# Optimization experiments

Measured on AMD Instinct MI355X. Metric: run time of the kernel, lower is better.

Reference implementation:

```python
import jax, jax.numpy as jnp
import numpy as np

B = 262144
MA = [128, 128]
MB = [128, 128]


def krone_linear(x_a, x_b, wa, wb, ba, bb):
    # slice inputs to each branch's in_features (torch slices the wider branch)
    ia, ib = wa.shape[1], wb.shape[1]
    x_a = x_a[:, :ia]
    x_b = x_b[:, :ib]
    h_a = x_a @ wa.T + ba
    h_b = x_b @ wb.T + bb
    # zero-pad the narrower output so both branches share a width (static shapes)
    oa, ob = wa.shape[0], wb.shape[0]
    if oa > ob:
        h_b = jnp.pad(h_b, ((0, 0), (0, oa - ob)))
    elif ob > oa:
        h_a = jnp.pad(h_a, ((0, 0), (0, ob - oa)))
    return h_a, h_b


def krone_softmax(x_a, x_b, fa, fb):
    x_a = x_a[:, :fa]
    x_b = x_b[:, :fb]
    # vectorized per-row Kronecker product: kron(a, b)[i*fb + j] = a[i]*b[j]
    y = (x_a[:, :, None] * x_b[:, None, :]).reshape(x_a.shape[0], fa * fb)
    return jax.nn.softmax(y, axis=1)


def setup_inputs() -> dict:
    key = jax.random.key(0)
    ks = jax.random.split(key, 13)
    s = 0.1
    inp = {
        "x": jax.random.normal(ks[0], (2, B, 2), dtype=jnp.float32),
        "w1a": jax.random.normal(ks[1], (MA[0], 2), dtype=jnp.float32) * s,
        "w1b": jax.random.normal(ks[2], (MB[0], 2), dtype=jnp.float32) * s,
        "b1a": jax.random.normal(ks[3], (MA[0],), dtype=jnp.float32) * s,
        "b1b": jax.random.normal(ks[4], (MB[0],), dtype=jnp.float32) * s,
        "w2a": jax.random.normal(ks[5], (MA[1], MA[0]), dtype=jnp.float32) * s,
        "w2b": jax.random.normal(ks[6], (MB[1], MB[0]), dtype=jnp.float32) * s,
        "b2a": jax.random.normal(ks[7], (MA[1],), dtype=jnp.float32) * s,
        "b2b": jax.random.normal(ks[8], (MB[1],), dtype=jnp.float32) * s,
        "w3a": jax.random.normal(ks[9], (1, MA[1]), dtype=jnp.float32) * s,
        "w3b": jax.random.normal(ks[10], (3, MB[1]), dtype=jnp.float32) * s,
        "b3a": jax.random.normal(ks[11], (1,), dtype=jnp.float32) * s,
        "b3b": jax.random.normal(ks[12], (3,), dtype=jnp.float32) * s,
    }
    return inp


def reference(x, w1a, w1b, b1a, b1b, w2a, w2b, b2a, b2b, w3a, w3b, b3a, b3b):
    x_a, x_b = x[0], x[1]
    h_a, h_b = krone_linear(x_a, x_b, w1a, w1b, b1a, b1b)
    h_a, h_b = jax.nn.relu(h_a), jax.nn.relu(h_b)
    h_a, h_b = krone_linear(h_a, h_b, w2a, w2b, b2a, b2b)
    h_a, h_b = jax.nn.relu(h_a), jax.nn.relu(h_b)
    h_a, h_b = krone_linear(h_a, h_b, w3a, w3b, b3a, b3b)
    return krone_softmax(h_a, h_b, 1, 3)
```

## Files before the change

kernel.cpp:

```cpp
#include <hip/hip_runtime.h>
#include <hip/hip_bf16.h>


#define BTOT 262144
#define NBLK (BTOT / 512)

typedef __attribute__((ext_vector_type(4))) float floatx4;
typedef __attribute__((ext_vector_type(8))) short bf16x8;
typedef __attribute__((ext_vector_type(4))) int  intx4;

#define OFF_W2   0
#define OFF_W1A  32768
#define OFF_W1B  35072
#define OFF_B2A  37376
#define OFF_B2B  37888
#define OFF_W3A  38400
#define OFF_W3T  38912
#define OFF_SA   40960
#define LDS_TOTAL 43008

static __device__ __forceinline__ int pack2bf(float lo, float hi) {
    int r;
    asm("v_cvt_pk_bf16_f32 %0, %1, %2" : "=v"(r) : "v"(lo), "v"(hi));
    return r;
}

template <int CTRL>
static __device__ __forceinline__ float dppadd(float v) {
    int t = __builtin_amdgcn_update_dpp(0, __builtin_bit_cast(int, v),
                                        CTRL, 0xF, 0xF, true);
    return v + __builtin_bit_cast(float, t);
}

static __device__ __forceinline__ float red4(float a0, float a1, float a2,
                                             float a3, int col) {
    float s0 = dppadd<0xB1>(a0), s1 = dppadd<0xB1>(a1);
    float s2 = dppadd<0xB1>(a2), s3 = dppadd<0xB1>(a3);
    float u0 = (col & 1) ? s1 : s0;
    float u1 = (col & 1) ? s3 : s2;
    float v0 = dppadd<0x4E>(u0), v1 = dppadd<0x4E>(u1);
    float w  = (col & 2) ? v1 : v0;
    w = dppadd<0x124>(w);
    w = dppadd<0x128>(w);
    return w;
}

static __device__ __forceinline__ int w1slot(int k) { return k + (k >> 3); }

static __device__ __forceinline__ void pack_w2(
        unsigned char* dst, int tid, const float* __restrict__ w2) {
    const float4* w2p = (const float4*)w2;
    #pragma unroll
    for (int i = 0; i < 8; ++i) {
        int n  = (tid & 15) | (i << 4);
        int k4 = tid >> 4;
        float4 f = w2p[n * 32 + k4];
        int k = k4 * 4;
        int s = k >> 5;
        int j0 = k & 7;
        int l = ((k & 31) >> 3) * 16 + (n & 15);
        int2 pkd;
        pkd.x = pack2bf(f.x, f.y);
        pkd.y = pack2bf(f.z, f.w);
        *(int2*)(dst + (s * 8 + (n >> 4)) * 1024 + l * 16 + j0 * 2) = pkd;
    }
}

static __device__ __forceinline__ void stage_small(
        unsigned char* smem, int tid, int offW1, int offB2,
        const float* __restrict__ w1, const float* __restrict__ b1,
        const float* __restrict__ b2) {
    if (tid < 128) {
        ((float4*)(smem + offW1))[w1slot(tid)] =
            make_float4(w1[2 * tid], w1[2 * tid + 1], b1[tid], 0.f);
        ((float*)(smem + offB2))[tid] = b2[tid];
    }
}

#define GEMM_CHUNK(acc, XV, W1p, W2p, B2p)                                     \
    {                                                                          \
        _Pragma("unroll")                                                      \
        for (int t = 0; t < 8; ++t) {                                          \
            float b2n = (B2p)[t * 16 + col];                                   \
            floatx4 bi = (floatx4){b2n, b2n, b2n, b2n};                        \
            _Pragma("unroll")                                                  \
            for (int mt = 0; mt < 2; ++mt) acc[t][mt] = bi;                    \
        }                                                                      \
        _Pragma("unroll")                                                      \
        for (int s = 0; s < 4; ++s) {                                          \
            intx4 af[2];                                                       \
            const int bslot = s * 36 + quad * 9;                               \
            _Pragma("unroll")                                                  \
            for (int j2 = 0; j2 < 4; ++j2) {                                   \
                float4 c0 = (W1p)[bslot + 2 * j2];                             \
                float4 c1 = (W1p)[bslot + 2 * j2 + 1];                         \
                _Pragma("unroll")                                              \
                for (int mt = 0; mt < 2; ++mt) {                               \
                    float h0 = fmaxf(fmaf((XV)[mt].x, c0.x,                    \
                                fmaf((XV)[mt].y, c0.y, c0.z)), 0.f);           \
                    float h1 = fmaxf(fmaf((XV)[mt].x, c1.x,                    \
                                fmaf((XV)[mt].y, c1.y, c1.z)), 0.f);           \
                    af[mt][j2] = pack2bf(h0, h1);                              \
                }                                                              \
            }                                                                  \
            _Pragma("unroll")                                                  \
            for (int t = 0; t < 8; ++t) {                                      \
                bf16x8 bfr = (W2p)[(s * 8 + t) * 64 + lane];                   \
                _Pragma("unroll")                                              \
                for (int mt = 0; mt < 2; ++mt)                                 \
                    acc[t][mt] = __builtin_amdgcn_mfma_f32_16x16x32_bf16(      \
                        __builtin_bit_cast(bf16x8, af[mt]), bfr,               \
                        acc[t][mt], 0, 0, 0);                                  \
            }                                                                  \
        }                                                                      \
    }

__global__ __launch_bounds__(512, 4)
void krone_fused(const float* __restrict__ x,
                 const float* __restrict__ w1a, const float* __restrict__ w1b,
                 const float* __restrict__ b1a, const float* __restrict__ b1b,
                 const float* __restrict__ w2a, const float* __restrict__ w2b,
                 const float* __restrict__ b2a, const float* __restrict__ b2b,
                 const float* __restrict__ w3a, const float* __restrict__ w3b,
                 const float* __restrict__ b3a, const float* __restrict__ b3b,
                 float* __restrict__ out) {
    __shared__ __align__(16) unsigned char smem[LDS_TOTAL];

    const int tid  = threadIdx.x;
    const int lane = tid & 63;
    const int wave = tid >> 6;
    const int quad = lane >> 4;
    const int col  = lane & 15;
    const int wbase = blockIdx.x * 512 + wave * 64;

    const bf16x8* W2  = (const bf16x8*)(smem + OFF_W2);
    const float4* W1A = (const float4*)(smem + OFF_W1A);
    const float4* W1B = (const float4*)(smem + OFF_W1B);
    const float*  B2A = (const float*)(smem + OFF_B2A);
    const float*  B2B = (const float*)(smem + OFF_B2B);
    const float*  W3A = (const float*)(smem + OFF_W3A);
    const floatx4* W3T = (const floatx4*)(smem + OFF_W3T);
    float*        SA  = (float*)(smem + OFF_SA);
    const float2* xA = (const float2*)x;
    const float2* xB = xA + BTOT;

    const float b3a_ = b3a[0];
    const float b30 = b3b[0], b31 = b3b[1], b32 = b3b[2];

    float2 xv[4];
    #pragma unroll
    for (int c = 0; c < 2; ++c)
        #pragma unroll
        for (int mt = 0; mt < 2; ++mt)
            xv[c * 2 + mt] = xA[wbase + c * 32 + mt * 16 + col];

    pack_w2(smem + OFF_W2, tid, w2a);
    stage_small(smem, tid, OFF_W1A, OFF_B2A, w1a, b1a, b2a);
    stage_small(smem, tid, OFF_W1B, OFF_B2B, w1b, b1b, b2b);
    if (tid < 128) ((float*)(smem + OFF_W3A))[tid] = w3a[tid];
    if (tid < 384) {
        int j = tid >> 7, n = tid & 127;
        ((float*)(smem + OFF_W3T))[n * 4 + j] = w3b[tid];
    }
    __syncthreads();

    #pragma unroll
    for (int c = 0; c < 2; ++c) {
        __builtin_amdgcn_sched_barrier(0);
        floatx4 acc[8][2];
        GEMM_CHUNK(acc, xv + 2 * c, W1A, W2, B2A);
        __builtin_amdgcn_sched_barrier(0);

        float pa[2][4] = {};
        #pragma unroll
        for (int t = 0; t < 8; ++t) {
            float w3n = W3A[t * 16 + col];
            #pragma unroll
            for (int mt = 0; mt < 2; ++mt)
                #pragma unroll
                for (int r = 0; r < 4; ++r)
                    pa[mt][r] = fmaf(w3n, fmaxf(acc[t][mt][r], 0.f), pa[mt][r]);
        }
        #pragma unroll
        for (int mt = 0; mt < 2; ++mt) {
            float w = red4(pa[mt][0], pa[mt][1], pa[mt][2], pa[mt][3], col);
            if (col < 4) {
                int sl = mt * 16 + quad * 4 + col;
                SA[wave * 64 + c * 32 + sl] = (w + b3a_) * 1.44269504089f;
            }
        }
        __builtin_amdgcn_sched_barrier(0);
    }

    #pragma unroll
    for (int c = 0; c < 2; ++c)
        #pragma unroll
        for (int mt = 0; mt < 2; ++mt)
            xv[c * 2 + mt] = xB[wbase + c * 32 + mt * 16 + col];

    __syncthreads();
    pack_w2(smem + OFF_W2, tid, w2b);
    __syncthreads();

    #pragma unroll
    for (int c = 0; c < 2; ++c) {
        __builtin_amdgcn_sched_barrier(0);
        floatx4 acc[8][2];
        GEMM_CHUNK(acc, xv + 2 * c, W1B, W2, B2B);
        __builtin_amdgcn_sched_barrier(0);

        #pragma unroll
        for (int mt = 0; mt < 2; ++mt) {
            float p0[4] = {}, p1[4] = {}, p2[4] = {};
            #pragma unroll
            for (int t = 0; t < 8; ++t) {
                floatx4 w3v = W3T[t * 16 + col];
                #pragma unroll
                for (int r = 0; r < 4; ++r) {
                    float h = fmaxf(acc[t][mt][r], 0.f);
                    p0[r] = fmaf(w3v.x, h, p0[r]);
                    p1[r] = fmaf(w3v.y, h, p1[r]);
                    p2[r] = fmaf(w3v.z, h, p2[r]);
                }
            }
            float t0 = red4(p0[0], p0[1], p0[2], p0[3], col) + b30;
            float t1 = red4(p1[0], p1[1], p1[2], p1[3], col) + b31;
            float t2 = red4(p2[0], p2[1], p2[2], p2[3], col) + b32;
            if (col < 4) {
                int sl = mt * 16 + quad * 4 + col;
                float sa = SA[wave * 64 + c * 32 + sl];
                float y0 = sa * t0, y1 = sa * t1, y2 = sa * t2;
                float m = fmaxf(y0, fmaxf(y1, y2));
                float e0 = exp2f(y0 - m), e1 = exp2f(y1 - m), e2 = exp2f(y2 - m);
                float rs = __builtin_amdgcn_rcpf(e0 + e1 + e2);
                long o = (long)(wbase + c * 32 + sl) * 3;
                out[o]     = e0 * rs;
                out[o + 1] = e1 * rs;
                out[o + 2] = e2 * rs;
            }
        }
        __builtin_amdgcn_sched_barrier(0);
    }
}

extern "C" void kernel_launch(void* const* d_in, const int* in_sizes, int n_in,
                              void* d_out, int out_size, void* d_ws, size_t ws_size,
                              hipStream_t stream) {
    const float* x   = (const float*)d_in[0];
    const float* w1a = (const float*)d_in[1];
    const float* w1b = (const float*)d_in[2];
    const float* b1a = (const float*)d_in[3];
    const float* b1b = (const float*)d_in[4];
    const float* w2a = (const float*)d_in[5];
    const float* w2b = (const float*)d_in[6];
    const float* b2a = (const float*)d_in[7];
    const float* b2b = (const float*)d_in[8];
    const float* w3a = (const float*)d_in[9];
    const float* w3b = (const float*)d_in[10];
    const float* b3a = (const float*)d_in[11];
    const float* b3b = (const float*)d_in[12];
    float* out = (float*)d_out;

    krone_fused<<<NBLK, 512, 0, stream>>>(x, w1a, w1b, b1a, b1b, w2a, w2b,
                                          b2a, b2b, w3a, w3b, b3a, b3b, out);
}
```

Before: 105.4 us.

## Compute first linear layer on MFMA with split-bf16 weights and inputs

Moves the first layer (2-input linear plus bias and ReLU) from scalar FMAs on LDS-staged float4 weights onto bf16 MFMA instructions. Weights, inputs and bias are each split into hi/lo bf16 parts so the product keeps near-fp32 accuracy, with bias folded in through a constant-one input element. The output fragment is laid out to feed the second GEMM's A operand directly. The aim is to cut VALU work in the inner loop, at the cost of extra MFMA issues and a larger LDS footprint for the expanded weight fragments.

```diff
diff --git a/kernel.cpp b/kernel.cpp
--- a/kernel.cpp
+++ b/kernel.cpp
@@ -9,15 +9,15 @@
 typedef __attribute__((ext_vector_type(8))) short bf16x8;
 typedef __attribute__((ext_vector_type(4))) int  intx4;
 
-#define OFF_W2   0
-#define OFF_W1A  32768
-#define OFF_W1B  35072
-#define OFF_B2A  37376
-#define OFF_B2B  37888
-#define OFF_W3A  38400
-#define OFF_W3T  38912
-#define OFF_SA   40960
-#define LDS_TOTAL 43008
+#define OFF_W2    0
+#define OFF_W1FA  32768
+#define OFF_W1FB  40960
+#define OFF_B2A   49152
+#define OFF_B2B   49664
+#define OFF_W3A   50176
+#define OFF_W3T   50688
+#define OFF_SA    52736
+#define LDS_TOTAL 54784
 
 static __device__ __forceinline__ int pack2bf(float lo, float hi) {
     int r;
@@ -44,8 +44,6 @@
     w = dppadd<0x128>(w);
     return w;
 }
-
-static __device__ __forceinline__ int w1slot(int k) { return k + (k >> 3); }
 
 static __device__ __forceinline__ void pack_w2(
         unsigned char* dst, int tid, const float* __restrict__ w2) {
@@ -66,18 +64,27 @@
     }
 }
 
-static __device__ __forceinline__ void stage_small(
-        unsigned char* smem, int tid, int offW1, int offB2,
-        const float* __restrict__ w1, const float* __restrict__ b1,
-        const float* __restrict__ b2) {
-    if (tid < 128) {
-        ((float4*)(smem + offW1))[w1slot(tid)] =
-            make_float4(w1[2 * tid], w1[2 * tid + 1], b1[tid], 0.f);
-        ((float*)(smem + offB2))[tid] = b2[tid];
-    }
-}
-
-#define GEMM_CHUNK(acc, XV, W1p, W2p, B2p)                                     \
+static __device__ __forceinline__ void stage_w1f(
+        unsigned char* smem, int off, int tid,
+        const float* __restrict__ w1, const float* __restrict__ b1) {
+    int tp = tid >> 6, l = tid & 63;
+    intx4 e = (intx4){0, 0, 0, 0};
+    if (l < 16) {
+        int n1 = (tp >> 1) * 32 + (l >> 2) * 8 + (tp & 1) * 4 + (l & 3);
+        float w0 = w1[2 * n1], w1v = w1[2 * n1 + 1], bb = b1[n1];
+        int dhi = pack2bf(w0, w1v);
+        float w0r = __builtin_bit_cast(float, dhi << 16);
+        float w1r = __builtin_bit_cast(float, dhi & 0xffff0000);
+        int dlo = pack2bf(w0 - w0r, w1v - w1r);
+        int bh  = pack2bf(bb, 0.f);
+        float bbr = __builtin_bit_cast(float, bh << 16);
+        int dbias = pack2bf(bb, bb - bbr);
+        e = (intx4){dhi, dlo, dhi, dbias};
+    }
+    ((intx4*)(smem + off))[tid] = e;
+}
+
+#define GEMM_CHUNK(acc, XF, W1Fp, W2p, B2p)                                    \
     {                                                                          \
         _Pragma("unroll")                                                      \
         for (int t = 0; t < 8; ++t) {                                          \
@@ -86,22 +93,22 @@
             _Pragma("unroll")                                                  \
             for (int mt = 0; mt < 2; ++mt) acc[t][mt] = bi;                    \
         }                                                                      \
+        const floatx4 zf = (floatx4){0.f, 0.f, 0.f, 0.f};                      \
         _Pragma("unroll")                                                      \
         for (int s = 0; s < 4; ++s) {                                          \
+            bf16x8 a0 = (W1Fp)[(2 * s) * 64 + lane];                           \
+            bf16x8 a1 = (W1Fp)[(2 * s + 1) * 64 + lane];                       \
             intx4 af[2];                                                       \
-            const int bslot = s * 36 + quad * 9;                               \
             _Pragma("unroll")                                                  \
-            for (int j2 = 0; j2 < 4; ++j2) {                                   \
-                float4 c0 = (W1p)[bslot + 2 * j2];                             \
-                float4 c1 = (W1p)[bslot + 2 * j2 + 1];                         \
-                _Pragma("unroll")                                              \
-                for (int mt = 0; mt < 2; ++mt) {                               \
-                    float h0 = fmaxf(fmaf((XV)[mt].x, c0.x,                    \
-                                fmaf((XV)[mt].y, c0.y, c0.z)), 0.f);           \
-                    float h1 = fmaxf(fmaf((XV)[mt].x, c1.x,                    \
-                                fmaf((XV)[mt].y, c1.y, c1.z)), 0.f);           \
-                    af[mt][j2] = pack2bf(h0, h1);                              \
-                }                                                              \
+            for (int mt = 0; mt < 2; ++mt) {                                   \
+                floatx4 td0 = __builtin_amdgcn_mfma_f32_16x16x32_bf16(         \
+                    a0, __builtin_bit_cast(bf16x8, (XF)[mt]), zf, 0, 0, 0);    \
+                floatx4 td1 = __builtin_amdgcn_mfma_f32_16x16x32_bf16(         \
+                    a1, __builtin_bit_cast(bf16x8, (XF)[mt]), zf, 0, 0, 0);    \
+                af[mt][0] = pack2bf(fmaxf(td0[0], 0.f), fmaxf(td0[1], 0.f));   \
+                af[mt][1] = pack2bf(fmaxf(td0[2], 0.f), fmaxf(td0[3], 0.f));   \
+                af[mt][2] = pack2bf(fmaxf(td1[0], 0.f), fmaxf(td1[1], 0.f));   \
+                af[mt][3] = pack2bf(fmaxf(td1[2], 0.f), fmaxf(td1[3], 0.f));   \
             }                                                                  \
             _Pragma("unroll")                                                  \
             for (int t = 0; t < 8; ++t) {                                      \
@@ -115,6 +122,14 @@
         }                                                                      \
     }
 
+static __device__ __forceinline__ intx4 make_xfrag(float2 xx) {
+    int d0 = pack2bf(xx.x, xx.y);
+    float r0 = __builtin_bit_cast(float, d0 << 16);
+    float r1 = __builtin_bit_cast(float, d0 & 0xffff0000);
+    int d2 = pack2bf(xx.x - r0, xx.y - r1);
+    return (intx4){d0, d0, d2, 0x3f803f80};
+}
+
 __global__ __launch_bounds__(512, 4)
 void krone_fused(const float* __restrict__ x,
                  const float* __restrict__ w1a, const float* __restrict__ w1b,
@@ -133,14 +148,14 @@
     const int col  = lane & 15;
     const int wbase = blockIdx.x * 512 + wave * 64;
 
-    const bf16x8* W2  = (const bf16x8*)(smem + OFF_W2);
-    const float4* W1A = (const float4*)(smem + OFF_W1A);
-    const float4* W1B = (const float4*)(smem + OFF_W1B);
-    const float*  B2A = (const float*)(smem + OFF_B2A);
-    const float*  B2B = (const float*)(smem + OFF_B2B);
-    const float*  W3A = (const float*)(smem + OFF_W3A);
+    const bf16x8* W2   = (const bf16x8*)(smem + OFF_W2);
+    const bf16x8* W1FA = (const bf16x8*)(smem + OFF_W1FA);
+    const bf16x8* W1FB = (const bf16x8*)(smem + OFF_W1FB);
+    const float*  B2A  = (const float*)(smem + OFF_B2A);
+    const float*  B2B  = (const float*)(smem + OFF_B2B);
+    const float*  W3A  = (const float*)(smem + OFF_W3A);
     const floatx4* W3T = (const floatx4*)(smem + OFF_W3T);
-    float*        SA  = (float*)(smem + OFF_SA);
+    float*        SA   = (float*)(smem + OFF_SA);
     const float2* xA = (const float2*)x;
     const float2* xB = xA + BTOT;
 
@@ -155,9 +170,13 @@
             xv[c * 2 + mt] = xA[wbase + c * 32 + mt * 16 + col];
 
     pack_w2(smem + OFF_W2, tid, w2a);
-    stage_small(smem, tid, OFF_W1A, OFF_B2A, w1a, b1a, b2a);
-    stage_small(smem, tid, OFF_W1B, OFF_B2B, w1b, b1b, b2b);
-    if (tid < 128) ((float*)(smem + OFF_W3A))[tid] = w3a[tid];
+    stage_w1f(smem, OFF_W1FA, tid, w1a, b1a);
+    stage_w1f(smem, OFF_W1FB, tid, w1b, b1b);
+    if (tid < 128) {
+        ((float*)(smem + OFF_B2A))[tid] = b2a[tid];
+        ((float*)(smem + OFF_B2B))[tid] = b2b[tid];
+        ((float*)(smem + OFF_W3A))[tid] = w3a[tid];
+    }
     if (tid < 384) {
         int j = tid >> 7, n = tid & 127;
         ((float*)(smem + OFF_W3T))[n * 4 + j] = w3b[tid];
@@ -167,8 +186,11 @@
     #pragma unroll
     for (int c = 0; c < 2; ++c) {
         __builtin_amdgcn_sched_barrier(0);
+        intx4 xf[2];
+        #pragma unroll
+        for (int mt = 0; mt < 2; ++mt) xf[mt] = make_xfrag(xv[c * 2 + mt]);
         floatx4 acc[8][2];
-        GEMM_CHUNK(acc, xv + 2 * c, W1A, W2, B2A);
+        GEMM_CHUNK(acc, xf, W1FA, W2, B2A);
         __builtin_amdgcn_sched_barrier(0);
 
         float pa[2][4] = {};
@@ -205,8 +227,11 @@
     #pragma unroll
     for (int c = 0; c < 2; ++c) {
         __builtin_amdgcn_sched_barrier(0);
+        intx4 xf[2];
+        #pragma unroll
+        for (int mt = 0; mt < 2; ++mt) xf[mt] = make_xfrag(xv[c * 2 + mt]);
         floatx4 acc[8][2];
-        GEMM_CHUNK(acc, xv + 2 * c, W1B, W2, B2B);
+        GEMM_CHUNK(acc, xf, W1FB, W2, B2B);
         __builtin_amdgcn_sched_barrier(0);
 
         #pragma unroll
```

Result: no change. 105.7 us (+0.3%).
